# Optimization experiments

Hardware: AMD Instinct MI355X
Metric: run time of the kernel (lower is better)

Reference implementation:

```python
import jax, jax.numpy as jnp
import numpy as np

B, X, Y, Z = 8, 128, 128, 128


def setup_inputs() -> dict:
    key = jax.random.key(0)
    k1, k2 = jax.random.split(key)
    mu = jax.random.normal(k1, (B, X, Y, Z), dtype=jnp.float32)
    active = jax.random.uniform(k2, (B, X, Y, Z), dtype=jnp.float32)
    dx = jnp.ones((1,), dtype=jnp.float32)
    return {"mu": mu, "active": active, "dx": dx}


def _lap_kernel(mu, active, dx):
    # mu, active: [X, Y, Z] single-sample grids; dx: scalar
    mu_eff = mu * active
    lap = (jnp.roll(mu_eff, 1, 0) + jnp.roll(mu_eff, -1, 0)
           + jnp.roll(mu_eff, 1, 1) + jnp.roll(mu_eff, -1, 1)
           + jnp.roll(mu_eff, 1, 2) + jnp.roll(mu_eff, -1, 2)
           - 6.0 * mu_eff) / dx ** 2
    return lap * active


def reference(mu, active, dx):
    # Faithful to Node.proces_collection: gather fields by pattern, then
    # vmap the runnable with in_axes=(0, 0, None) over the batch axis.
    out = jax.vmap(_lap_kernel, in_axes=(0, 0, None))(mu, active, dx[0])
    return out
```

## Files before the change

kernel.cpp:

```cpp
#include <hip/hip_runtime.h>

#define NB 8
#define NX 128
#define NY 128
#define NZ 128

#define TY 16
#define TX 16
#define XC (NX / TX)
#define YT (NY / TY)
#define ROWS (TY + 2)

__global__ __launch_bounds__(512) void lap_march(
    const float* __restrict__ mu,
    const float* __restrict__ act,
    const float* __restrict__ dxp,
    float* __restrict__ out)
{
    __shared__ float buf[2][ROWS][NZ];

    const int tid = threadIdx.x;
    const int bid = blockIdx.x;
    const int xc = bid & (XC - 1);
    const int yt = (bid >> 3) & (YT - 1);
    const int b  = bid >> 6;

    const int x0 = xc * TX;
    const int y0 = yt * TY;
    const int planeYZ = NY * NZ;
    const int baseB = b * NX * planeYZ;

    const float dxv = dxp[0];
    const float inv = 1.0f / (dxv * dxv);

    const int r  = tid >> 5;
    const int zq = tid & 31;
    const int z0 = zq * 4;
    const int gy = y0 + r;

    float4 eP, eC, eN, aC, aN;

    auto ldE = [&](int gx, float4* ev, float4* av) {
        const int gIdx = baseB + gx * planeYZ + gy * NZ + z0;
        float4 m = *reinterpret_cast<const float4*>(mu + gIdx);
        float4 a = *reinterpret_cast<const float4*>(act + gIdx);
        *av = a;
        *ev = make_float4(m.x * a.x, m.y * a.y, m.z * a.z, m.w * a.w);
    };

    auto ldHalo = [&](int gx, int slot) {
        if (tid < 64) {
            const int hr = tid >> 5;
            const int hz = (tid & 31) * 4;
            const int hy = hr ? ((y0 + TY) & (NY - 1)) : ((y0 - 1) & (NY - 1));
            const int gIdx = baseB + gx * planeYZ + hy * NZ + hz;
            float4 m = *reinterpret_cast<const float4*>(mu + gIdx);
            float4 a = *reinterpret_cast<const float4*>(act + gIdx);
            *reinterpret_cast<float4*>(&buf[slot][hr ? TY + 1 : 0][hz]) =
                make_float4(m.x * a.x, m.y * a.y, m.z * a.z, m.w * a.w);
        }
    };

    {
        float4 dummy;
        ldE((x0 - 1) & (NX - 1), &eP, &dummy);
        ldE(x0, &eC, &aC);
        *reinterpret_cast<float4*>(&buf[0][r + 1][z0]) = eC;
        ldHalo(x0, 0);
    }
    __syncthreads();

    for (int i = 0; i < TX; ++i) {
        const int gxn = (x0 + i + 1) & (NX - 1);
        ldE(gxn, &eN, &aN);
        if (i < TX - 1) {
            *reinterpret_cast<float4*>(&buf[(i + 1) & 1][r + 1][z0]) = eN;
            ldHalo(gxn, (i + 1) & 1);
        }

        const int s = i & 1;
        float4 eym = *reinterpret_cast<const float4*>(&buf[s][r][z0]);
        float4 eyp = *reinterpret_cast<const float4*>(&buf[s][r + 2][z0]);
        float ezm = __shfl(eC.w, (zq + 31) & 31, 32);
        float ezp = __shfl(eC.x, (zq + 1) & 31, 32);

        float4 o;
        o.x = (eP.x + eN.x + eym.x + eyp.x + ezm  + eC.y - 6.0f * eC.x) * inv * aC.x;
        o.y = (eP.y + eN.y + eym.y + eyp.y + eC.x + eC.z - 6.0f * eC.y) * inv * aC.y;
        o.z = (eP.z + eN.z + eym.z + eyp.z + eC.y + eC.w - 6.0f * eC.z) * inv * aC.z;
        o.w = (eP.w + eN.w + eym.w + eyp.w + eC.z + ezp  - 6.0f * eC.w) * inv * aC.w;

        const int gIdx = baseB + (x0 + i) * planeYZ + gy * NZ + z0;
        *reinterpret_cast<float4*>(out + gIdx) = o;

        eP = eC; eC = eN; aC = aN;
        __syncthreads();
    }
}

extern "C" void kernel_launch(void* const* d_in, const int* in_sizes, int n_in,
                              void* d_out, int out_size, void* d_ws, size_t ws_size,
                              hipStream_t stream) {
    const float* mu  = (const float*)d_in[0];
    const float* act = (const float*)d_in[1];
    const float* dx  = (const float*)d_in[2];
    float* out = (float*)d_out;

    const int grid = NB * YT * XC;
    lap_march<<<grid, 512, 0, stream>>>(mu, act, dx, out);
}
```

Baseline: 36.10 us.

## Prefetch next-next x-plane in registers and halve x-march length

Loads for plane x+2 are now issued one iteration ahead, held in registers, and multiplied only when consumed. The aim is to keep a global load in flight across each barrier and hide memory latency. The march tile along x is also halved, which doubles the number of blocks for more parallelism. In exchange, each block re-reads a larger share of redundant neighbour planes, and the extra prefetch registers increase register use.

Result: slower. 39.20 us (+8.6%).

```diff
diff --git a/kernel.cpp b/kernel.cpp
--- a/kernel.cpp
+++ b/kernel.cpp
@@ -6,12 +6,15 @@
 #define NZ 128
 
 #define TY 16
-#define TX 16
+#define TX 8
 #define XC (NX / TX)
 #define YT (NY / TY)
 #define ROWS (TY + 2)
 
-__global__ __launch_bounds__(512) void lap_march(
+#define EMUL(e, m, a) \
+    e.x = m.x * a.x; e.y = m.y * a.y; e.z = m.z * a.z; e.w = m.w * a.w;
+
+__global__ __launch_bounds__(512) void lap_pipe(
     const float* __restrict__ mu,
     const float* __restrict__ act,
     const float* __restrict__ dxp,
@@ -22,8 +25,8 @@
     const int tid = threadIdx.x;
     const int bid = blockIdx.x;
     const int xc = bid & (XC - 1);
-    const int yt = (bid >> 3) & (YT - 1);
-    const int b  = bid >> 6;
+    const int yt = (bid >> 4) & (YT - 1);
+    const int b  = bid >> 7;
 
     const int x0 = xc * TX;
     const int y0 = yt * TY;
@@ -37,45 +40,58 @@
     const int zq = tid & 31;
     const int z0 = zq * 4;
     const int gy = y0 + r;
+    const int rowOff = gy * NZ + z0;
 
-    float4 eP, eC, eN, aC, aN;
+    const int hr   = tid >> 5;
+    const int hy   = hr ? ((y0 + TY) & (NY - 1)) : ((y0 - 1) & (NY - 1));
+    const int hRow = hr ? (TY + 1) : 0;
+    const int hOff = hy * NZ + z0;
 
-    auto ldE = [&](int gx, float4* ev, float4* av) {
-        const int gIdx = baseB + gx * planeYZ + gy * NZ + z0;
-        float4 m = *reinterpret_cast<const float4*>(mu + gIdx);
-        float4 a = *reinterpret_cast<const float4*>(act + gIdx);
-        *av = a;
-        *ev = make_float4(m.x * a.x, m.y * a.y, m.z * a.z, m.w * a.w);
-    };
+    float4 eP, eC, aC;
+    float4 mN, aN;
+    float4 mNN, aNN;
+    float4 hm, ha, hmNN, haNN;
 
-    auto ldHalo = [&](int gx, int slot) {
-        if (tid < 64) {
-            const int hr = tid >> 5;
-            const int hz = (tid & 31) * 4;
-            const int hy = hr ? ((y0 + TY) & (NY - 1)) : ((y0 - 1) & (NY - 1));
-            const int gIdx = baseB + gx * planeYZ + hy * NZ + hz;
-            float4 m = *reinterpret_cast<const float4*>(mu + gIdx);
-            float4 a = *reinterpret_cast<const float4*>(act + gIdx);
-            *reinterpret_cast<float4*>(&buf[slot][hr ? TY + 1 : 0][hz]) =
-                make_float4(m.x * a.x, m.y * a.y, m.z * a.z, m.w * a.w);
-        }
+    auto ld = [&](int gx, int off, float4* m, float4* a) {
+        const int gIdx = baseB + gx * planeYZ + off;
+        *m = *reinterpret_cast<const float4*>(mu + gIdx);
+        *a = *reinterpret_cast<const float4*>(act + gIdx);
     };
 
     {
-        float4 dummy;
-        ldE((x0 - 1) & (NX - 1), &eP, &dummy);
-        ldE(x0, &eC, &aC);
+        float4 m0, a0;
+        ld((x0 - 1) & (NX - 1), rowOff, &m0, &a0);
+        EMUL(eP, m0, a0);
+        ld(x0, rowOff, &m0, &aC);
+        EMUL(eC, m0, aC);
         *reinterpret_cast<float4*>(&buf[0][r + 1][z0]) = eC;
-        ldHalo(x0, 0);
+        if (tid < 64) {
+            float4 m1, a1, e1;
+            ld(x0, hOff, &m1, &a1);
+            EMUL(e1, m1, a1);
+            *reinterpret_cast<float4*>(&buf[0][hRow][z0]) = e1;
+        }
+        ld((x0 + 1) & (NX - 1), rowOff, &mN, &aN);
+        if (tid < 64) ld((x0 + 1) & (NX - 1), hOff, &hm, &ha);
+        __syncthreads();
     }
-    __syncthreads();
 
     for (int i = 0; i < TX; ++i) {
-        const int gxn = (x0 + i + 1) & (NX - 1);
-        ldE(gxn, &eN, &aN);
+        if (i < TX - 1) {
+            const int gx2 = (x0 + i + 2) & (NX - 1);
+            ld(gx2, rowOff, &mNN, &aNN);
+            if (tid < 64) ld(gx2, hOff, &hmNN, &haNN);
+        }
+
+        float4 eN;
+        EMUL(eN, mN, aN);
         if (i < TX - 1) {
             *reinterpret_cast<float4*>(&buf[(i + 1) & 1][r + 1][z0]) = eN;
-            ldHalo(gxn, (i + 1) & 1);
+            if (tid < 64) {
+                float4 he;
+                EMUL(he, hm, ha);
+                *reinterpret_cast<float4*>(&buf[(i + 1) & 1][hRow][z0]) = he;
+            }
         }
 
         const int s = i & 1;
@@ -90,10 +106,12 @@
         o.z = (eP.z + eN.z + eym.z + eyp.z + eC.y + eC.w - 6.0f * eC.z) * inv * aC.z;
         o.w = (eP.w + eN.w + eym.w + eyp.w + eC.z + ezp  - 6.0f * eC.w) * inv * aC.w;
 
-        const int gIdx = baseB + (x0 + i) * planeYZ + gy * NZ + z0;
+        const int gIdx = baseB + (x0 + i) * planeYZ + rowOff;
         *reinterpret_cast<float4*>(out + gIdx) = o;
 
         eP = eC; eC = eN; aC = aN;
+        mN = mNN; aN = aNN; hm = hmNN; ha = haNN;
+
         __syncthreads();
     }
 }
@@ -107,5 +125,5 @@
     float* out = (float*)d_out;
 
     const int grid = NB * YT * XC;
-    lap_march<<<grid, 512, 0, stream>>>(mu, act, dx, out);
+    lap_pipe<<<grid, 512, 0, stream>>>(mu, act, dx, out);
 }
```
